# Optimization experiments

Hardware: AMD Instinct MI355X
Metric: run time of the kernel (lower is better)

The kernel has to match this reference:

```python
import jax, jax.numpy as jnp
import numpy as np

B = 8192   # batch of trajectories
T = 32     # time points
H = 256    # hidden_dim
NL = 4     # num_layers
EPS = 1e-5 # LayerNorm eps (torch default)


def setup_inputs() -> dict:
    key = jax.random.key(0)
    ks = jax.random.split(key, 8)
    # xavier-ish scales (gain 0.5 for hidden, 0.1 for output, per _init_weights)
    s0 = 0.5 * np.sqrt(2.0 / (6 + H))
    sh = 0.5 * np.sqrt(2.0 / (H + H))
    so = 0.1 * np.sqrt(2.0 / (H + 3))
    return {
        "y0": jax.random.normal(ks[0], (B, 3), dtype=jnp.float32),
        "t_span": jnp.arange(T, dtype=jnp.float32) * 0.01,
        "params": jax.random.uniform(ks[1], (B, 3), dtype=jnp.float32),  # [Omega, Delta, gamma] > 0
        "W0": jax.random.normal(ks[2], (6, H), dtype=jnp.float32) * s0,
        "b0": jnp.zeros((H,), dtype=jnp.float32),
        "Wh": jax.random.normal(ks[3], (NL - 1, H, H), dtype=jnp.float32) * sh,
        "bh": jnp.zeros((NL - 1, H), dtype=jnp.float32),
        "ln_g": jnp.ones((NL, H), dtype=jnp.float32),
        "ln_b": jnp.zeros((NL, H), dtype=jnp.float32),
        "Wout": jax.random.normal(ks[4], (H, 3), dtype=jnp.float32) * so,
        "bout": jnp.zeros((3,), dtype=jnp.float32),
        "gate": jnp.float32(0.5),
    }


def _layernorm(h, g, b):
    mu = jnp.mean(h, axis=-1, keepdims=True)
    var = jnp.mean(jnp.square(h - mu), axis=-1, keepdims=True)
    return (h - mu) * jax.lax.rsqrt(var + EPS) * g + b


def reference(y0, t_span, params, W0, b0, Wh, bh, ln_g, ln_b, Wout, bout, gate):
    def correction_net(y, p):
        # input: concat([u,v,w, Omega,Delta,gamma]) -> (B, 6)
        h = jnp.concatenate([y, p], axis=-1) @ W0 + b0
        h = jax.nn.silu(_layernorm(h, ln_g[0], ln_b[0]))
        for i in range(NL - 1):
            h = jax.nn.silu(_layernorm(h @ Wh[i] + bh[i], ln_g[i + 1], ln_b[i + 1]))
        return h @ Wout + bout  # (B, 3)

    def bloch_rhs_incomplete(y, p):
        u, v, w = y[:, 0:1], y[:, 1:2], y[:, 2:3]
        Om, ga = p[:, 0:1], p[:, 2:3]
        du = -ga * u
        dv = -ga * v - Om * w
        dw = -2.0 * ga * (w + 1.0) + Om * v
        return jnp.concatenate([du, dv, dw], axis=-1)

    def f_total(y):
        return bloch_rhs_incomplete(y, params) + gate * correction_net(y, params)

    def rk4_step(y, dt):
        k1 = f_total(y)
        k2 = f_total(y + 0.5 * dt * k1)
        k3 = f_total(y + 0.5 * dt * k2)
        k4 = f_total(y + dt * k3)
        y_new = y + (dt / 6.0) * (k1 + 2.0 * k2 + 2.0 * k3 + k4)
        return y_new, y_new

    dts = jnp.diff(t_span)              # (T-1,)
    _, ys = jax.lax.scan(rk4_step, y0, dts)
    return jnp.concatenate([y0[None], ys], axis=0)  # (T, B, 3)
```

## Files before the change

kernel.cpp:

```cpp
#include <hip/hip_runtime.h>

typedef unsigned short u16;
typedef unsigned int   u32;
typedef short v8s   __attribute__((ext_vector_type(8)));
typedef float f32x4 __attribute__((ext_vector_type(4)));
typedef float f32x2 __attribute__((ext_vector_type(2)));

#define H_ 256
#define B_ 8192
#define NSTEP 31
#define NTHREADS 512
#define NBLOCKS 256
#define AROW 264

#define MFMA16(a,b,c) __builtin_amdgcn_mfma_f32_16x16x32_bf16(a,b,c,0,0,0)

#define DPP_QP_XOR1 0xB1
#define DPP_QP_XOR2 0x4E
#define DPP_ROR4    0x124
#define DPP_ROR8    0x128

template<int CTRL>
__device__ __forceinline__ float dpp_add(float v){
  return v + __int_as_float(__builtin_amdgcn_update_dpp(0, __float_as_int(v), CTRL, 0xF, 0xF, true));
}
template<int CTRL>
__device__ __forceinline__ float dpp_mov(float v){
  return __int_as_float(__builtin_amdgcn_update_dpp(0, __float_as_int(v), CTRL, 0xF, 0xF, true));
}

__device__ __forceinline__ u16 f2bf_rne(float f){
  unsigned u = __float_as_uint(f);
  u += 0x7fffu + ((u >> 16) & 1u);
  return (u16)(u >> 16);
}
__device__ __forceinline__ u16 f2bf_trunc(float f){
  return (u16)(__float_as_uint(f) >> 16);
}

#define WS_W0   0
#define WS_W1   8192
#define WS_W23  73728
#define WS_TOT  204800

__global__ void prep_kernel(const float* __restrict__ W0,
                            const float* __restrict__ b0,
                            const float* __restrict__ Wh,
                            u16* __restrict__ ws){
  int i = blockIdx.x * 256 + threadIdx.x;
  if (i < 8192){
    int q = i >> 11, n = (i >> 3) & 255, j = i & 7;
    int k = q*8 + j;
    float v = (k < 6) ? W0[k*H_ + n] : ((k == 6) ? b0[n] : 0.f);
    ws[i] = f2bf_rne(v);
  } else if (i < 73728){
    int r = i - 8192;
    int n = r >> 8, k = r & 255;
    ws[i] = f2bf_rne(Wh[k*H_ + n]);
  } else if (i < WS_TOT){
    int r = i - 73728;
    int j = r & 7, kc = (r >> 3) & 7, col = (r >> 6) & 255;
    int q = (r >> 14) & 3, l = (r >> 16) & 1;
    int k = kc*32 + q*8 + j;
    ws[i] = f2bf_rne(Wh[(1 + l)*H_*H_ + k*H_ + col]);
  }
}

#define PWF 20
#define OFF_A      0
#define OFF_W1     16896
#define OFF_PART   152064
#define OFF_NETP   154624
#define OFF_DTS    158720
#define LDS_TOTAL  158848

__global__ __launch_bounds__(NTHREADS, 2)
void pinode_kernel(const float* __restrict__ y0g, const float* __restrict__ t_span,
                   const float* __restrict__ params, const float* __restrict__ bhg,
                   const float* __restrict__ ln_gg, const float* __restrict__ ln_bg,
                   const float* __restrict__ boutg, const float* __restrict__ gatep,
                   const float* __restrict__ Woutg, const u16* __restrict__ ws,
                   float* __restrict__ out)
{
  extern __shared__ char smem[];
  u16*   A     = (u16*)(smem + OFF_A);
  u16*   W1    = (u16*)(smem + OFF_W1);
  float* partf = (float*)(smem + OFF_PART);
  float* netp  = (float*)(smem + OFF_NETP);
  float* dts   = (float*)(smem + OFF_DTS);

  const int tid  = threadIdx.x;
  const int wave = tid >> 6;
  const int lane = tid & 63;
  const int q    = lane >> 4;
  const int c15  = lane & 15;
  const int cg   = wave;
  const int colbase = cg * 32;
  const int s0 = blockIdx.x * 32;
  const bool oddl = (c15 & 1);

  for (int idx = tid; idx < 8192; idx += NTHREADS){
    int n = idx >> 5, ch = idx & 31;
    *(v8s*)(W1 + n*AROW + ch*8) = *(const v8s*)(ws + WS_W1 + n*256 + ch*8);
  }
  if (tid < NSTEP) dts[tid] = t_span[tid+1] - t_span[tid];

  float yc0=0,yc1=0,yc2=0, ys0=0,ys1=0,ys2=0, su0=0,su1=0,su2=0, Om=0,P1=0,ga=0;
  if (tid < 32){
    int s = tid;
    yc0 = y0g[(s0+s)*3+0]; yc1 = y0g[(s0+s)*3+1]; yc2 = y0g[(s0+s)*3+2];
    Om  = params[(s0+s)*3+0]; P1 = params[(s0+s)*3+1]; ga = params[(s0+s)*3+2];
    ys0 = yc0; ys1 = yc1; ys2 = yc2;
    out[(s0+s)*3+0] = yc0; out[(s0+s)*3+1] = yc1; out[(s0+s)*3+2] = yc2;
    union { u16 h[8]; v8s v; } pk;
    pk.h[0]=f2bf_rne(yc0); pk.h[1]=f2bf_rne(yc1); pk.h[2]=f2bf_rne(yc2);
    pk.h[3]=f2bf_rne(Om);  pk.h[4]=f2bf_rne(P1);  pk.h[5]=f2bf_rne(ga);
    pk.h[6]=0x3F80; pk.h[7]=0;
    *(v8s*)(A + s*AROW) = pk.v;
    v8s z = {0,0,0,0,0,0,0,0};
    *(v8s*)(A + s*AROW + 8)  = z;
    *(v8s*)(A + s*AROW + 16) = z;
    *(v8s*)(A + s*AROW + 24) = z;
  }
  const float gate = gatep[0];
  const float bo0 = boutg[0], bo1 = boutg[1], bo2 = boutg[2];

  v8s w0f[2];
#pragma unroll
  for (int nt = 0; nt < 2; ++nt)
    w0f[nt] = *(const v8s*)(ws + WS_W0 + (q*256 + colbase + nt*16 + c15)*8);

  v8s wf[2][8][2];
#pragma unroll
  for (int l = 0; l < 2; ++l)
#pragma unroll
    for (int nt = 0; nt < 2; ++nt)
#pragma unroll
      for (int kc = 0; kc < 8; ++kc)
        wf[l][kc][nt] = *(const v8s*)(ws + WS_W23 +
            ((l*4 + q)*256 + colbase + nt*16 + c15)*64 + kc*8);

  float wo[2][3];
#pragma unroll
  for (int nt = 0; nt < 2; ++nt)
#pragma unroll
    for (int o = 0; o < 3; ++o)
      wo[nt][o] = Woutg[(colbase + nt*16 + c15)*3 + o];

  float lng[4][2], lnb[4][2], bia[3][2];
#pragma unroll
  for (int l = 0; l < 4; ++l)
#pragma unroll
    for (int nt = 0; nt < 2; ++nt){
      int col = colbase + nt*16 + c15;
      lng[l][nt] = ln_gg[l*H_ + col];
      lnb[l][nt] = ln_bg[l*H_ + col];
      if (l >= 1) bia[l-1][nt] = bhg[(l-1)*H_ + col];
    }

  const u16* pa = A  + c15*AROW + q*8;
  const u16* pw = W1 + (colbase + c15)*AROW + q*8;
  const f32x4 fzero = {0.f,0.f,0.f,0.f};
  const int storecol = colbase + c15 + (oddl ? 15 : 0);

  __syncthreads();

  auto ln_head = [&](f32x4 (&acc)[2][2], float (&sr)[2][4], float (&sb)[2][4]){
    float rs[2][4], rq[2][4];
#pragma unroll
    for (int mt = 0; mt < 2; ++mt)
#pragma unroll
      for (int r = 0; r < 4; ++r){
        float a0 = acc[mt][0][r], a1 = acc[mt][1][r];
        rs[mt][r] = a0 + a1;
        rq[mt][r] = a0*a0 + a1*a1;
      }
#pragma unroll
    for (int mt = 0; mt < 2; ++mt)
#pragma unroll
      for (int r = 0; r < 4; ++r){
        float s = rs[mt][r], qq = rq[mt][r];
        s = dpp_add<DPP_QP_XOR1>(s);  qq = dpp_add<DPP_QP_XOR1>(qq);
        s = dpp_add<DPP_QP_XOR2>(s);  qq = dpp_add<DPP_QP_XOR2>(qq);
        s = dpp_add<DPP_ROR4>(s);     qq = dpp_add<DPP_ROR4>(qq);
        s = dpp_add<DPP_ROR8>(s);     qq = dpp_add<DPP_ROR8>(qq);
        rs[mt][r] = s; rq[mt][r] = qq;
      }
    if (c15 < 4){
#pragma unroll
      for (int mt = 0; mt < 2; ++mt){
        float sS = (c15==0) ? rs[mt][0] : (c15==1) ? rs[mt][1] : (c15==2) ? rs[mt][2] : rs[mt][3];
        float sQ = (c15==0) ? rq[mt][0] : (c15==1) ? rq[mt][1] : (c15==2) ? rq[mt][2] : rq[mt][3];
        f32x2 v; v.x = sS; v.y = sQ;
        *(f32x2*)(partf + (mt*16 + q*4 + c15)*PWF + cg*2) = v;
      }
    }
    __syncthreads();
    int l32 = lane & 31;
    const f32x4* pp = (const f32x4*)(partf + l32*PWF);
    f32x4 p0 = pp[0], p1 = pp[1], p2 = pp[2], p3 = pp[3];
    float S = ((p0[0]+p0[2])+(p1[0]+p1[2]))+((p2[0]+p2[2])+(p3[0]+p3[2]));
    float Q = ((p0[1]+p0[3])+(p1[1]+p1[3]))+((p2[1]+p2[3])+(p3[1]+p3[3]));
    float mean = S * (1.f/256.f);
    float var  = Q * (1.f/256.f) - mean*mean;
    float rstd = rsqrtf(var + 1e-5f);
    float nmr  = -mean * rstd;
#pragma unroll
    for (int mt = 0; mt < 2; ++mt)
#pragma unroll
      for (int r = 0; r < 4; ++r){
        int row = mt*16 + q*4 + r;
        sr[mt][r] = __int_as_float(__builtin_amdgcn_ds_bpermute(row << 2, __float_as_int(rstd)));
        sb[mt][r] = __int_as_float(__builtin_amdgcn_ds_bpermute(row << 2, __float_as_int(nmr)));
      }
  };

  auto ln_mid = [&](f32x4 (&acc)[2][2], int li){
    float sr[2][4], sb[2][4];
    ln_head(acc, sr, sb);
    float g0 = lng[li][0], b0_ = lnb[li][0];
    float g1 = lng[li][1], b1_ = lnb[li][1];
#pragma unroll
    for (int mt = 0; mt < 2; ++mt)
#pragma unroll
      for (int r = 0; r < 4; ++r){
        float t0 = acc[mt][0][r]*sr[mt][r] + sb[mt][r];
        float t1 = acc[mt][1][r]*sr[mt][r] + sb[mt][r];
        float v0 = t0*g0 + b0_;
        float v1 = t1*g1 + b1_;
        float sv0 = v0 * __builtin_amdgcn_rcpf(1.f + __builtin_amdgcn_exp2f(v0 * -1.44269504f));
        float sv1 = v1 * __builtin_amdgcn_rcpf(1.f + __builtin_amdgcn_exp2f(v1 * -1.44269504f));
        float send = oddl ? sv0 : sv1;
        float recv = dpp_mov<DPP_QP_XOR1>(send);
        float lo = oddl ? recv : sv0;
        float hi = oddl ? sv1 : recv;
        u32 word = (u32)f2bf_trunc(lo) | ((u32)f2bf_trunc(hi) << 16);
        *(u32*)(A + (mt*16 + q*4 + r)*AROW + storecol) = word;
      }
    __syncthreads();
  };

#pragma unroll 1
  for (int step = 0; step < NSTEP; ++step){
    float dt = 0.f;
    if (tid < 32) dt = dts[step];
#pragma unroll 1
    for (int stage = 0; stage < 4; ++stage){
      f32x4 acc[2][2];

#pragma unroll
      for (int mt = 0; mt < 2; ++mt){ acc[mt][0] = fzero; acc[mt][1] = fzero; }
      {
        v8s a0 = *(const v8s*)(pa);
        v8s a1 = *(const v8s*)(pa + 16*AROW);
        acc[0][0] = MFMA16(a0, w0f[0], acc[0][0]);
        acc[0][1] = MFMA16(a0, w0f[1], acc[0][1]);
        acc[1][0] = MFMA16(a1, w0f[0], acc[1][0]);
        acc[1][1] = MFMA16(a1, w0f[1], acc[1][1]);
      }
      ln_mid(acc, 0);

#pragma unroll
      for (int mt = 0; mt < 2; ++mt){ acc[mt][0] = fzero; acc[mt][1] = fzero; }
#pragma unroll
      for (int kc = 0; kc < 8; ++kc){
        v8s a0  = *(const v8s*)(pa + kc*32);
        v8s a1  = *(const v8s*)(pa + 16*AROW + kc*32);
        v8s b0f = *(const v8s*)(pw + kc*32);
        v8s b1f = *(const v8s*)(pw + 16*AROW + kc*32);
        acc[0][0] = MFMA16(a0, b0f, acc[0][0]);
        acc[0][1] = MFMA16(a0, b1f, acc[0][1]);
        acc[1][0] = MFMA16(a1, b0f, acc[1][0]);
        acc[1][1] = MFMA16(a1, b1f, acc[1][1]);
      }
#pragma unroll
      for (int mt = 0; mt < 2; ++mt)
#pragma unroll
        for (int nt = 0; nt < 2; ++nt)
#pragma unroll
          for (int r = 0; r < 4; ++r) acc[mt][nt][r] += bia[0][nt];
      ln_mid(acc, 1);

#pragma unroll
      for (int l = 0; l < 2; ++l){
#pragma unroll
        for (int mt = 0; mt < 2; ++mt){ acc[mt][0] = fzero; acc[mt][1] = fzero; }
#pragma unroll
        for (int kc = 0; kc < 8; ++kc){
          v8s a0 = *(const v8s*)(pa + kc*32);
          v8s a1 = *(const v8s*)(pa + 16*AROW + kc*32);
          acc[0][0] = MFMA16(a0, wf[l][kc][0], acc[0][0]);
          acc[0][1] = MFMA16(a0, wf[l][kc][1], acc[0][1]);
          acc[1][0] = MFMA16(a1, wf[l][kc][0], acc[1][0]);
          acc[1][1] = MFMA16(a1, wf[l][kc][1], acc[1][1]);
        }
#pragma unroll
        for (int mt = 0; mt < 2; ++mt)
#pragma unroll
          for (int nt = 0; nt < 2; ++nt)
#pragma unroll
            for (int r = 0; r < 4; ++r) acc[mt][nt][r] += bia[1+l][nt];
        if (l == 0) ln_mid(acc, 2);
      }

      {
        float sr[2][4], sb[2][4];
        ln_head(acc, sr, sb);
        float g0 = lng[3][0], b0_ = lnb[3][0];
        float g1 = lng[3][1], b1_ = lnb[3][1];
#pragma unroll
        for (int mt = 0; mt < 2; ++mt)
#pragma unroll
          for (int r = 0; r < 4; ++r){
            float t0 = acc[mt][0][r]*sr[mt][r] + sb[mt][r];
            float t1 = acc[mt][1][r]*sr[mt][r] + sb[mt][r];
            float v0 = t0*g0 + b0_;
            float v1 = t1*g1 + b1_;
            float sv0 = v0 * __builtin_amdgcn_rcpf(1.f + __builtin_amdgcn_exp2f(v0 * -1.44269504f));
            float sv1 = v1 * __builtin_amdgcn_rcpf(1.f + __builtin_amdgcn_exp2f(v1 * -1.44269504f));
            float po0 = sv0*wo[0][0] + sv1*wo[1][0];
            float po1 = sv0*wo[0][1] + sv1*wo[1][1];
            float po2 = sv0*wo[0][2] + sv1*wo[1][2];
            po0 = dpp_add<DPP_QP_XOR1>(po0); po1 = dpp_add<DPP_QP_XOR1>(po1); po2 = dpp_add<DPP_QP_XOR1>(po2);
            po0 = dpp_add<DPP_QP_XOR2>(po0); po1 = dpp_add<DPP_QP_XOR2>(po1); po2 = dpp_add<DPP_QP_XOR2>(po2);
            po0 = dpp_add<DPP_ROR4>(po0);    po1 = dpp_add<DPP_ROR4>(po1);    po2 = dpp_add<DPP_ROR4>(po2);
            po0 = dpp_add<DPP_ROR8>(po0);    po1 = dpp_add<DPP_ROR8>(po1);    po2 = dpp_add<DPP_ROR8>(po2);
            if (c15 == 0){
              f32x4 st; st[0] = po0; st[1] = po1; st[2] = po2; st[3] = 0.f;
              *(f32x4*)(netp + (cg*32 + mt*16 + q*4 + r)*4) = st;
            }
          }
      }
      __syncthreads();

      if (tid < 32){
        int s = tid;
        float n0 = 0.f, n1 = 0.f, n2 = 0.f;
#pragma unroll
        for (int c = 0; c < 8; ++c){
          f32x4 v = *(const f32x4*)(netp + (c*32 + s)*4);
          n0 += v[0]; n1 += v[1]; n2 += v[2];
        }
        float k0 = -ga*ys0                      + gate*(n0 + bo0);
        float k1 = -ga*ys1 - Om*ys2             + gate*(n1 + bo1);
        float k2 = -2.f*ga*(ys2 + 1.f) + Om*ys1 + gate*(n2 + bo2);
        if (stage == 0){
          su0 = yc0 + dt*(1.f/6.f)*k0; su1 = yc1 + dt*(1.f/6.f)*k1; su2 = yc2 + dt*(1.f/6.f)*k2;
          ys0 = yc0 + 0.5f*dt*k0; ys1 = yc1 + 0.5f*dt*k1; ys2 = yc2 + 0.5f*dt*k2;
        } else if (stage == 1){
          su0 += dt*(1.f/3.f)*k0; su1 += dt*(1.f/3.f)*k1; su2 += dt*(1.f/3.f)*k2;
          ys0 = yc0 + 0.5f*dt*k0; ys1 = yc1 + 0.5f*dt*k1; ys2 = yc2 + 0.5f*dt*k2;
        } else if (stage == 2){
          su0 += dt*(1.f/3.f)*k0; su1 += dt*(1.f/3.f)*k1; su2 += dt*(1.f/3.f)*k2;
          ys0 = yc0 + dt*k0; ys1 = yc1 + dt*k1; ys2 = yc2 + dt*k2;
        } else {
          yc0 = su0 + dt*(1.f/6.f)*k0; yc1 = su1 + dt*(1.f/6.f)*k1; yc2 = su2 + dt*(1.f/6.f)*k2;
          ys0 = yc0; ys1 = yc1; ys2 = yc2;
          out[(step+1)*(B_*3) + (s0+s)*3 + 0] = yc0;
          out[(step+1)*(B_*3) + (s0+s)*3 + 1] = yc1;
          out[(step+1)*(B_*3) + (s0+s)*3 + 2] = yc2;
        }
        union { u16 h[8]; v8s v; } pk;
        pk.h[0]=f2bf_rne(ys0); pk.h[1]=f2bf_rne(ys1); pk.h[2]=f2bf_rne(ys2);
        pk.h[3]=f2bf_rne(Om);  pk.h[4]=f2bf_rne(P1);  pk.h[5]=f2bf_rne(ga);
        pk.h[6]=0x3F80; pk.h[7]=0;
        *(v8s*)(A + s*AROW) = pk.v;
      }
      __syncthreads();
    }
  }
}

extern "C" void kernel_launch(void* const* d_in, const int* in_sizes, int n_in,
                              void* d_out, int out_size, void* d_ws, size_t ws_size,
                              hipStream_t stream) {
  const float* y0     = (const float*)d_in[0];
  const float* t_span = (const float*)d_in[1];
  const float* params = (const float*)d_in[2];
  const float* W0     = (const float*)d_in[3];
  const float* b0     = (const float*)d_in[4];
  const float* Wh     = (const float*)d_in[5];
  const float* bh     = (const float*)d_in[6];
  const float* ln_g   = (const float*)d_in[7];
  const float* ln_b   = (const float*)d_in[8];
  const float* Wout   = (const float*)d_in[9];
  const float* bout   = (const float*)d_in[10];
  const float* gate   = (const float*)d_in[11];
  float* out = (float*)d_out;
  u16* ws = (u16*)d_ws;

  prep_kernel<<<WS_TOT/256, 256, 0, stream>>>(W0, b0, Wh, ws);

  hipFuncSetAttribute(reinterpret_cast<const void*>(pinode_kernel),
                      hipFuncAttributeMaxDynamicSharedMemorySize, LDS_TOTAL);
  pinode_kernel<<<NBLOCKS, NTHREADS, LDS_TOTAL, stream>>>(
      y0, t_span, params, bh, ln_g, ln_b, bout, gate, Wout, ws, out);
}
```

Baseline: 1.244 ms.

## Replicate RK4 state per wave and build layer-0 fragments via bpermute

Every wave now keeps the 32 trajectory states redundantly and builds the layer-0 MFMA A fragments in registers with ds_bpermute, instead of one wave writing them to LDS. This drops a block-wide barrier per RK stage. LayerNorm statistics go to a per-wave LDS slot instead of being broadcast by bpermute, the bias is folded into the accumulator init, and the bf16 packing uses byte-perm with packed float2 math. In exchange, state updates are done redundantly in all waves, layer-0 inputs use truncating bf16 conversion, and the hidden-layer loop is no longer unrolled.

```diff
diff --git a/kernel.cpp b/kernel.cpp
--- a/kernel.cpp
+++ b/kernel.cpp
@@ -25,17 +25,16 @@
   return v + __int_as_float(__builtin_amdgcn_update_dpp(0, __float_as_int(v), CTRL, 0xF, 0xF, true));
 }
 template<int CTRL>
-__device__ __forceinline__ float dpp_mov(float v){
-  return __int_as_float(__builtin_amdgcn_update_dpp(0, __float_as_int(v), CTRL, 0xF, 0xF, true));
-}
-
+__device__ __forceinline__ u32 dpp_movu(u32 v){
+  return (u32)__builtin_amdgcn_update_dpp(0, (int)v, CTRL, 0xF, 0xF, true);
+}
+__device__ __forceinline__ u32 permb(u32 a, u32 b, u32 sel){
+  return __builtin_amdgcn_perm(a, b, sel);
+}
 __device__ __forceinline__ u16 f2bf_rne(float f){
   unsigned u = __float_as_uint(f);
   u += 0x7fffu + ((u >> 16) & 1u);
   return (u16)(u >> 16);
-}
-__device__ __forceinline__ u16 f2bf_trunc(float f){
-  return (u16)(__float_as_uint(f) >> 16);
 }
 
 #define WS_W0   0
@@ -71,8 +70,9 @@
 #define OFF_W1     16896
 #define OFF_PART   152064
 #define OFF_NETP   154624
-#define OFF_DTS    158720
-#define LDS_TOTAL  158848
+#define OFF_MRS    158720
+#define OFF_DTS    160768
+#define LDS_TOTAL  160896
 
 __global__ __launch_bounds__(NTHREADS, 2)
 void pinode_kernel(const float* __restrict__ y0g, const float* __restrict__ t_span,
@@ -87,6 +87,7 @@
   u16*   W1    = (u16*)(smem + OFF_W1);
   float* partf = (float*)(smem + OFF_PART);
   float* netp  = (float*)(smem + OFF_NETP);
+  float* mrsA  = (float*)(smem + OFF_MRS);
   float* dts   = (float*)(smem + OFF_DTS);
 
   const int tid  = threadIdx.x;
@@ -94,10 +95,12 @@
   const int lane = tid & 63;
   const int q    = lane >> 4;
   const int c15  = lane & 15;
+  const int l32  = lane & 31;
   const int cg   = wave;
   const int colbase = cg * 32;
   const int s0 = blockIdx.x * 32;
   const bool oddl = (c15 & 1);
+  const u32  xsel = oddl ? 0x07060302u : 0x01000504u;
 
   for (int idx = tid; idx < 8192; idx += NTHREADS){
     int n = idx >> 5, ch = idx & 31;
@@ -105,22 +108,15 @@
   }
   if (tid < NSTEP) dts[tid] = t_span[tid+1] - t_span[tid];
 
-  float yc0=0,yc1=0,yc2=0, ys0=0,ys1=0,ys2=0, su0=0,su1=0,su2=0, Om=0,P1=0,ga=0;
-  if (tid < 32){
-    int s = tid;
+  float yc0,yc1,yc2, ys0,ys1,ys2, su0=0,su1=0,su2=0, Om,P1,ga;
+  {
+    int s = l32;
     yc0 = y0g[(s0+s)*3+0]; yc1 = y0g[(s0+s)*3+1]; yc2 = y0g[(s0+s)*3+2];
     Om  = params[(s0+s)*3+0]; P1 = params[(s0+s)*3+1]; ga = params[(s0+s)*3+2];
     ys0 = yc0; ys1 = yc1; ys2 = yc2;
-    out[(s0+s)*3+0] = yc0; out[(s0+s)*3+1] = yc1; out[(s0+s)*3+2] = yc2;
-    union { u16 h[8]; v8s v; } pk;
-    pk.h[0]=f2bf_rne(yc0); pk.h[1]=f2bf_rne(yc1); pk.h[2]=f2bf_rne(yc2);
-    pk.h[3]=f2bf_rne(Om);  pk.h[4]=f2bf_rne(P1);  pk.h[5]=f2bf_rne(ga);
-    pk.h[6]=0x3F80; pk.h[7]=0;
-    *(v8s*)(A + s*AROW) = pk.v;
-    v8s z = {0,0,0,0,0,0,0,0};
-    *(v8s*)(A + s*AROW + 8)  = z;
-    *(v8s*)(A + s*AROW + 16) = z;
-    *(v8s*)(A + s*AROW + 24) = z;
+    if (wave == 0 && lane < 32){
+      out[(s0+s)*3+0] = yc0; out[(s0+s)*3+1] = yc1; out[(s0+s)*3+2] = yc2;
+    }
   }
   const float gate = gatep[0];
   const float bo0 = boutg[0], bo1 = boutg[1], bo2 = boutg[2];
@@ -147,25 +143,44 @@
     for (int o = 0; o < 3; ++o)
       wo[nt][o] = Woutg[(colbase + nt*16 + c15)*3 + o];
 
-  float lng[4][2], lnb[4][2], bia[3][2];
-#pragma unroll
-  for (int l = 0; l < 4; ++l)
-#pragma unroll
-    for (int nt = 0; nt < 2; ++nt){
-      int col = colbase + nt*16 + c15;
-      lng[l][nt] = ln_gg[l*H_ + col];
-      lnb[l][nt] = ln_bg[l*H_ + col];
-      if (l >= 1) bia[l-1][nt] = bhg[(l-1)*H_ + col];
-    }
+  f32x2 lg2[4], lb2[4];
+  float bia[3][2];
+#pragma unroll
+  for (int l = 0; l < 4; ++l){
+    int c0 = colbase + c15, c1 = colbase + 16 + c15;
+    lg2[l].x = ln_gg[l*H_ + c0]; lg2[l].y = ln_gg[l*H_ + c1];
+    lb2[l].x = ln_bg[l*H_ + c0]; lb2[l].y = ln_bg[l*H_ + c1];
+    if (l >= 1){ bia[l-1][0] = bhg[(l-1)*H_ + c0]; bia[l-1][1] = bhg[(l-1)*H_ + c1]; }
+  }
 
   const u16* pa = A  + c15*AROW + q*8;
   const u16* pw = W1 + (colbase + c15)*AROW + q*8;
+  u16* pst2 = A + colbase + (oddl ? 16 : 0) + (c15 & ~1);
+  float* mymrs = mrsA + wave*64;
   const f32x4 fzero = {0.f,0.f,0.f,0.f};
-  const int storecol = colbase + c15 + (oddl ? 15 : 0);
+  const int ba0 = c15 << 2, ba1 = (16 + c15) << 2;
+
+  v8s fa0, fa1;
+  u32 p2c = permb(__float_as_uint(ga), __float_as_uint(P1), 0x07060302u);
+  auto build_frags = [&](){
+    u32 p0 = permb(__float_as_uint(ys1), __float_as_uint(ys0), 0x07060302u);
+    u32 p1 = permb(__float_as_uint(Om),  __float_as_uint(ys2), 0x07060302u);
+    union { u32 w[4]; v8s v; } f0, f1;
+    f0.w[0] = (u32)__builtin_amdgcn_ds_bpermute(ba0, (int)p0);
+    f0.w[1] = (u32)__builtin_amdgcn_ds_bpermute(ba0, (int)p1);
+    f0.w[2] = (u32)__builtin_amdgcn_ds_bpermute(ba0, (int)p2c);
+    f0.w[3] = 0x00003F80u;
+    f1.w[0] = (u32)__builtin_amdgcn_ds_bpermute(ba1, (int)p0);
+    f1.w[1] = (u32)__builtin_amdgcn_ds_bpermute(ba1, (int)p1);
+    f1.w[2] = (u32)__builtin_amdgcn_ds_bpermute(ba1, (int)p2c);
+    f1.w[3] = 0x00003F80u;
+    fa0 = f0.v; fa1 = f1.v;
+  };
+  build_frags();
 
   __syncthreads();
 
-  auto ln_head = [&](f32x4 (&acc)[2][2], float (&sr)[2][4], float (&sb)[2][4]){
+  auto ln_head = [&](f32x4 (&acc)[2][2]){
     float rs[2][4], rq[2][4];
 #pragma unroll
     for (int mt = 0; mt < 2; ++mt)
@@ -196,7 +211,6 @@
       }
     }
     __syncthreads();
-    int l32 = lane & 31;
     const f32x4* pp = (const f32x4*)(partf + l32*PWF);
     f32x4 p0 = pp[0], p1 = pp[1], p2 = pp[2], p3 = pp[3];
     float S = ((p0[0]+p0[2])+(p1[0]+p1[2]))+((p2[0]+p2[2])+(p3[0]+p3[2]));
@@ -204,64 +218,60 @@
     float mean = S * (1.f/256.f);
     float var  = Q * (1.f/256.f) - mean*mean;
     float rstd = rsqrtf(var + 1e-5f);
-    float nmr  = -mean * rstd;
+    if (lane < 32){
+      f32x2 mr; mr.x = rstd; mr.y = -mean*rstd;
+      *(f32x2*)(mymrs + l32*2) = mr;
+    }
+  };
+
+  auto ln_tail = [&](f32x4 (&acc)[2][2], int li){
+    f32x2 g2 = lg2[li], b2 = lb2[li];
 #pragma unroll
     for (int mt = 0; mt < 2; ++mt)
 #pragma unroll
       for (int r = 0; r < 4; ++r){
-        int row = mt*16 + q*4 + r;
-        sr[mt][r] = __int_as_float(__builtin_amdgcn_ds_bpermute(row << 2, __float_as_int(rstd)));
-        sb[mt][r] = __int_as_float(__builtin_amdgcn_ds_bpermute(row << 2, __float_as_int(nmr)));
-      }
-  };
-
-  auto ln_mid = [&](f32x4 (&acc)[2][2], int li){
-    float sr[2][4], sb[2][4];
-    ln_head(acc, sr, sb);
-    float g0 = lng[li][0], b0_ = lnb[li][0];
-    float g1 = lng[li][1], b1_ = lnb[li][1];
-#pragma unroll
-    for (int mt = 0; mt < 2; ++mt)
-#pragma unroll
-      for (int r = 0; r < 4; ++r){
-        float t0 = acc[mt][0][r]*sr[mt][r] + sb[mt][r];
-        float t1 = acc[mt][1][r]*sr[mt][r] + sb[mt][r];
-        float v0 = t0*g0 + b0_;
-        float v1 = t1*g1 + b1_;
-        float sv0 = v0 * __builtin_amdgcn_rcpf(1.f + __builtin_amdgcn_exp2f(v0 * -1.44269504f));
-        float sv1 = v1 * __builtin_amdgcn_rcpf(1.f + __builtin_amdgcn_exp2f(v1 * -1.44269504f));
-        float send = oddl ? sv0 : sv1;
-        float recv = dpp_mov<DPP_QP_XOR1>(send);
-        float lo = oddl ? recv : sv0;
-        float hi = oddl ? sv1 : recv;
-        u32 word = (u32)f2bf_trunc(lo) | ((u32)f2bf_trunc(hi) << 16);
-        *(u32*)(A + (mt*16 + q*4 + r)*AROW + storecol) = word;
+        f32x2 mr = *(const f32x2*)(mymrs + (mt*16 + q*4 + r)*2);
+        f32x2 sc = g2 * mr.x;
+        f32x2 of = g2 * mr.y + b2;
+        f32x2 av; av.x = acc[mt][0][r]; av.y = acc[mt][1][r];
+        f32x2 v  = av * sc + of;
+        f32x2 ea = v * (-1.44269504f);
+        f32x2 den; den.x = 1.f + __builtin_amdgcn_exp2f(ea.x);
+                   den.y = 1.f + __builtin_amdgcn_exp2f(ea.y);
+        f32x2 rc; rc.x = __builtin_amdgcn_rcpf(den.x); rc.y = __builtin_amdgcn_rcpf(den.y);
+        f32x2 sv = v * rc;
+        u32 own = permb(__float_as_uint(sv.y), __float_as_uint(sv.x), 0x07060302u);
+        u32 par = dpp_movu<DPP_QP_XOR1>(own);
+        u32 word = permb(own, par, xsel);
+        *(u32*)(pst2 + (mt*16 + q*4 + r)*AROW) = word;
       }
     __syncthreads();
   };
 
 #pragma unroll 1
   for (int step = 0; step < NSTEP; ++step){
-    float dt = 0.f;
-    if (tid < 32) dt = dts[step];
+    float dt = dts[step];
 #pragma unroll 1
     for (int stage = 0; stage < 4; ++stage){
       f32x4 acc[2][2];
 
 #pragma unroll
       for (int mt = 0; mt < 2; ++mt){ acc[mt][0] = fzero; acc[mt][1] = fzero; }
-      {
-        v8s a0 = *(const v8s*)(pa);
-        v8s a1 = *(const v8s*)(pa + 16*AROW);
-        acc[0][0] = MFMA16(a0, w0f[0], acc[0][0]);
-        acc[0][1] = MFMA16(a0, w0f[1], acc[0][1]);
-        acc[1][0] = MFMA16(a1, w0f[0], acc[1][0]);
-        acc[1][1] = MFMA16(a1, w0f[1], acc[1][1]);
-      }
-      ln_mid(acc, 0);
-
-#pragma unroll
-      for (int mt = 0; mt < 2; ++mt){ acc[mt][0] = fzero; acc[mt][1] = fzero; }
+      acc[0][0] = MFMA16(fa0, w0f[0], acc[0][0]);
+      acc[0][1] = MFMA16(fa0, w0f[1], acc[0][1]);
+      acc[1][0] = MFMA16(fa1, w0f[0], acc[1][0]);
+      acc[1][1] = MFMA16(fa1, w0f[1], acc[1][1]);
+      ln_head(acc);
+      ln_tail(acc, 0);
+
+#pragma unroll
+      for (int mt = 0; mt < 2; ++mt)
+#pragma unroll
+        for (int nt = 0; nt < 2; ++nt){
+          float b = bia[0][nt];
+          f32x4 bb; bb[0]=b; bb[1]=b; bb[2]=b; bb[3]=b;
+          acc[mt][nt] = bb;
+        }
 #pragma unroll
       for (int kc = 0; kc < 8; ++kc){
         v8s a0  = *(const v8s*)(pa + kc*32);
@@ -273,18 +283,19 @@
         acc[1][0] = MFMA16(a1, b0f, acc[1][0]);
         acc[1][1] = MFMA16(a1, b1f, acc[1][1]);
       }
-#pragma unroll
-      for (int mt = 0; mt < 2; ++mt)
-#pragma unroll
-        for (int nt = 0; nt < 2; ++nt)
-#pragma unroll
-          for (int r = 0; r < 4; ++r) acc[mt][nt][r] += bia[0][nt];
-      ln_mid(acc, 1);
-
-#pragma unroll
+      ln_head(acc);
+      ln_tail(acc, 1);
+
+#pragma unroll 1
       for (int l = 0; l < 2; ++l){
 #pragma unroll
-        for (int mt = 0; mt < 2; ++mt){ acc[mt][0] = fzero; acc[mt][1] = fzero; }
+        for (int mt = 0; mt < 2; ++mt)
+#pragma unroll
+          for (int nt = 0; nt < 2; ++nt){
+            float b = bia[1+l][nt];
+            f32x4 bb; bb[0]=b; bb[1]=b; bb[2]=b; bb[3]=b;
+            acc[mt][nt] = bb;
+          }
 #pragma unroll
         for (int kc = 0; kc < 8; ++kc){
           v8s a0 = *(const v8s*)(pa + kc*32);
@@ -294,33 +305,29 @@
           acc[1][0] = MFMA16(a1, wf[l][kc][0], acc[1][0]);
           acc[1][1] = MFMA16(a1, wf[l][kc][1], acc[1][1]);
         }
+        if (l == 0){ ln_head(acc); ln_tail(acc, 2); }
+      }
+
+      {
+        ln_head(acc);
+        f32x2 g2 = lg2[3], b2 = lb2[3];
 #pragma unroll
         for (int mt = 0; mt < 2; ++mt)
 #pragma unroll
-          for (int nt = 0; nt < 2; ++nt)
-#pragma unroll
-            for (int r = 0; r < 4; ++r) acc[mt][nt][r] += bia[1+l][nt];
-        if (l == 0) ln_mid(acc, 2);
-      }
-
-      {
-        float sr[2][4], sb[2][4];
-        ln_head(acc, sr, sb);
-        float g0 = lng[3][0], b0_ = lnb[3][0];
-        float g1 = lng[3][1], b1_ = lnb[3][1];
-#pragma unroll
-        for (int mt = 0; mt < 2; ++mt)
-#pragma unroll
           for (int r = 0; r < 4; ++r){
-            float t0 = acc[mt][0][r]*sr[mt][r] + sb[mt][r];
-            float t1 = acc[mt][1][r]*sr[mt][r] + sb[mt][r];
-            float v0 = t0*g0 + b0_;
-            float v1 = t1*g1 + b1_;
-            float sv0 = v0 * __builtin_amdgcn_rcpf(1.f + __builtin_amdgcn_exp2f(v0 * -1.44269504f));
-            float sv1 = v1 * __builtin_amdgcn_rcpf(1.f + __builtin_amdgcn_exp2f(v1 * -1.44269504f));
-            float po0 = sv0*wo[0][0] + sv1*wo[1][0];
-            float po1 = sv0*wo[0][1] + sv1*wo[1][1];
-            float po2 = sv0*wo[0][2] + sv1*wo[1][2];
+            f32x2 mr = *(const f32x2*)(mymrs + (mt*16 + q*4 + r)*2);
+            f32x2 sc = g2 * mr.x;
+            f32x2 of = g2 * mr.y + b2;
+            f32x2 av; av.x = acc[mt][0][r]; av.y = acc[mt][1][r];
+            f32x2 v  = av * sc + of;
+            f32x2 ea = v * (-1.44269504f);
+            f32x2 den; den.x = 1.f + __builtin_amdgcn_exp2f(ea.x);
+                       den.y = 1.f + __builtin_amdgcn_exp2f(ea.y);
+            f32x2 rc; rc.x = __builtin_amdgcn_rcpf(den.x); rc.y = __builtin_amdgcn_rcpf(den.y);
+            f32x2 sv = v * rc;
+            float po0 = sv.x*wo[0][0] + sv.y*wo[1][0];
+            float po1 = sv.x*wo[0][1] + sv.y*wo[1][1];
+            float po2 = sv.x*wo[0][2] + sv.y*wo[1][2];
             po0 = dpp_add<DPP_QP_XOR1>(po0); po1 = dpp_add<DPP_QP_XOR1>(po1); po2 = dpp_add<DPP_QP_XOR1>(po2);
             po0 = dpp_add<DPP_QP_XOR2>(po0); po1 = dpp_add<DPP_QP_XOR2>(po1); po2 = dpp_add<DPP_QP_XOR2>(po2);
             po0 = dpp_add<DPP_ROR4>(po0);    po1 = dpp_add<DPP_ROR4>(po1);    po2 = dpp_add<DPP_ROR4>(po2);
@@ -333,8 +340,8 @@
       }
       __syncthreads();
 
-      if (tid < 32){
-        int s = tid;
+      {
+        int s = l32;
         float n0 = 0.f, n1 = 0.f, n2 = 0.f;
 #pragma unroll
         for (int c = 0; c < 8; ++c){
@@ -356,17 +363,14 @@
         } else {
           yc0 = su0 + dt*(1.f/6.f)*k0; yc1 = su1 + dt*(1.f/6.f)*k1; yc2 = su2 + dt*(1.f/6.f)*k2;
           ys0 = yc0; ys1 = yc1; ys2 = yc2;
-          out[(step+1)*(B_*3) + (s0+s)*3 + 0] = yc0;
-          out[(step+1)*(B_*3) + (s0+s)*3 + 1] = yc1;
-          out[(step+1)*(B_*3) + (s0+s)*3 + 2] = yc2;
+          if (wave == 0 && lane < 32){
+            out[(step+1)*(B_*3) + (s0+s)*3 + 0] = yc0;
+            out[(step+1)*(B_*3) + (s0+s)*3 + 1] = yc1;
+            out[(step+1)*(B_*3) + (s0+s)*3 + 2] = yc2;
+          }
         }
-        union { u16 h[8]; v8s v; } pk;
-        pk.h[0]=f2bf_rne(ys0); pk.h[1]=f2bf_rne(ys1); pk.h[2]=f2bf_rne(ys2);
-        pk.h[3]=f2bf_rne(Om);  pk.h[4]=f2bf_rne(P1);  pk.h[5]=f2bf_rne(ga);
-        pk.h[6]=0x3F80; pk.h[7]=0;
-        *(v8s*)(A + s*AROW) = pk.v;
-      }
-      __syncthreads();
+        build_frags();
+      }
     }
   }
 }
```

Result: slower. 2.063 ms (+65.9%).
